# Kernel optimization log

Hardware: AMD Instinct MI355X
Metric: run time of the kernel (lower is better)

The kernel has to match this reference:

```python
import jax, jax.numpy as jnp
import numpy as np

N = 50000      # num nodes
E = 800000     # num edges (avg degree 16)
LAGS = 16      # in_channels of the cell input
FILT = 64      # hidden filters
K = 2          # diffusion steps
CIN = LAGS + FILT  # DConv input channels (cat of x and hidden)


def _dconv(X, row, col, norm_out, norm_in, W, b):
    """Diffusion conv, K=2. W: (2, K, Cin, Cout), b: (Cout,).
    Hop 0: identity for both directions. Hop 1: out-diffusion (D_O^-1 A) and
    in-diffusion (D_I^-1 A^T) via gather-scale-scatter."""
    H = X @ W[0, 0] + X @ W[1, 0]
    # out-direction: message along edge (row -> col), aggregated at col
    Tx_o = jax.ops.segment_sum(norm_out[:, None] * X[row], col, num_segments=N)
    # in-direction: reversed edges (col -> row), aggregated at row
    Tx_i = jax.ops.segment_sum(norm_in[:, None] * X[col], row, num_segments=N)
    H = H + Tx_o @ W[0, 1] + Tx_i @ W[1, 1]
    return H + b


def setup_inputs() -> dict:
    key = jax.random.key(0)
    ks = jax.random.split(key, 12)
    scale = 1.0 / np.sqrt(CIN)
    inp = {
        "x": jax.random.normal(ks[0], (N, LAGS), dtype=jnp.float32),
        "edge_index": jax.random.randint(ks[1], (2, E), 0, N, dtype=jnp.int64),
        "edge_weight": jax.random.uniform(ks[2], (E,), dtype=jnp.float32),
        "w_z": jax.random.uniform(ks[3], (2, K, CIN, FILT), jnp.float32, -scale, scale),
        "b_z": jnp.zeros((FILT,), jnp.float32),
        "w_r": jax.random.uniform(ks[4], (2, K, CIN, FILT), jnp.float32, -scale, scale),
        "b_r": jnp.zeros((FILT,), jnp.float32),
        "w_h": jax.random.uniform(ks[5], (2, K, CIN, FILT), jnp.float32, -scale, scale),
        "b_h": jnp.zeros((FILT,), jnp.float32),
        "lin_w": jax.random.uniform(ks[6], (FILT, 1), jnp.float32, -1.0 / np.sqrt(FILT), 1.0 / np.sqrt(FILT)),
        "lin_b": jnp.zeros((1,), jnp.float32),
    }
    return inp


def reference(x, edge_index, edge_weight, w_z, b_z, w_r, b_r, w_h, b_h, lin_w, lin_b):
    row, col = edge_index[0], edge_index[1]
    # weighted out/in degrees (original builds a dense adj just for these)
    deg_out = jax.ops.segment_sum(edge_weight, row, num_segments=N)
    deg_in = jax.ops.segment_sum(edge_weight, col, num_segments=N)
    deg_out = jnp.where(deg_out > 0, deg_out, 1.0)  # unused entries guarded
    deg_in = jnp.where(deg_in > 0, deg_in, 1.0)
    norm_out = (1.0 / deg_out)[row]
    norm_in = (1.0 / deg_in)[col]

    H0 = jnp.zeros((x.shape[0], FILT), dtype=x.dtype)  # hidden state init
    XH = jnp.concatenate([x, H0], axis=1)
    Z = jax.nn.sigmoid(_dconv(XH, row, col, norm_out, norm_in, w_z, b_z))
    R = jax.nn.sigmoid(_dconv(XH, row, col, norm_out, norm_in, w_r, b_r))
    XRH = jnp.concatenate([x, R * H0], axis=1)
    H_tilde = jnp.tanh(_dconv(XRH, row, col, norm_out, norm_in, w_h, b_h))
    H = Z * H0 + (1.0 - Z) * H_tilde
    h = jax.nn.relu(H)
    return h @ lin_w + lin_b  # [N, 1]
```

## Files before the change

kernel.cpp:

```cpp
#include <hip/hip_runtime.h>
#include <math.h>

#define N_NODES 50000
#define N_EDGES 800000
#define LAGS 16
#define FILT 64
#define W00_OFF 0
#define W01_OFF (80*64)
#define W10_OFF (2*80*64)
#define W11_OFF (3*80*64)

__device__ __forceinline__ void atomAddF(float* p, float v) {
    unsafeAtomicAdd(p, v);
}

__global__ __launch_bounds__(256) void deg_kernel(
    const int* __restrict__ row, const int* __restrict__ col,
    const float* __restrict__ ew,
    float* __restrict__ deg_out, float* __restrict__ deg_in)
{
    for (int e = blockIdx.x * 256 + threadIdx.x; e < N_EDGES;
         e += gridDim.x * 256) {
        float w = ew[e];
        atomAddF(&deg_out[row[e]], w);
        atomAddF(&deg_in[col[e]], w);
    }
}

__global__ __launch_bounds__(256) void scale_kernel(
    const float* __restrict__ x,
    const float* __restrict__ deg_out, const float* __restrict__ deg_in,
    float* __restrict__ Xs_o, float* __restrict__ Xs_i)
{
    for (int n = blockIdx.x * 256 + threadIdx.x; n < N_NODES;
         n += gridDim.x * 256) {
        float d_o = deg_out[n];
        float d_i = deg_in[n];
        float io = (d_o > 0.0f) ? (1.0f / d_o) : 1.0f;
        float ii = (d_i > 0.0f) ? (1.0f / d_i) : 1.0f;
        const float4* px = (const float4*)(x + (size_t)n * LAGS);
        float4* po = (float4*)(Xs_o + (size_t)n * LAGS);
        float4* pi = (float4*)(Xs_i + (size_t)n * LAGS);
#pragma unroll
        for (int q = 0; q < 4; ++q) {
            float4 v = px[q];
            po[q] = make_float4(io * v.x, io * v.y, io * v.z, io * v.w);
            pi[q] = make_float4(ii * v.x, ii * v.y, ii * v.z, ii * v.w);
        }
    }
}

__global__ __launch_bounds__(256) void scatter_kernel(
    const int* __restrict__ row, const int* __restrict__ col,
    const float* __restrict__ Xs_o, const float* __restrict__ Xs_i,
    float* __restrict__ Tx_o, float* __restrict__ Tx_i)
{
    const int total = N_EDGES * 16;
    for (int t = blockIdx.x * 256 + threadIdx.x; t < total;
         t += gridDim.x * 256) {
        int e  = t >> 4;
        int ch = t & 15;
        int r = row[e], c = col[e];
        float vo = Xs_o[(size_t)r * LAGS + ch];
        float vi = Xs_i[(size_t)c * LAGS + ch];
        atomAddF(&Tx_o[(size_t)c * LAGS + ch], vo);
        atomAddF(&Tx_i[(size_t)r * LAGS + ch], vi);
    }
}

__global__ __launch_bounds__(256) void node_kernel(
    const float* __restrict__ x,
    const float* __restrict__ Tx_o, const float* __restrict__ Tx_i,
    const float* __restrict__ w_z, const float* __restrict__ b_z,
    const float* __restrict__ w_h, const float* __restrict__ b_h,
    const float* __restrict__ lin_w, const float* __restrict__ lin_b,
    float* __restrict__ out)
{
    __shared__ float Wzc[FILT * 16], Wzo[FILT * 16], Wzi[FILT * 16];
    __shared__ float Whc[FILT * 16], Who[FILT * 16], Whi[FILT * 16];
    __shared__ float sbz[FILT], sbh[FILT], slw[FILT];

    const int tid = threadIdx.x;
    for (int i = tid; i < FILT * 16; i += 256) {
        int c = i >> 6, f = i & 63;
        int t = f * 16 + c;
        int g = c * 64 + f;
        Wzc[t] = w_z[W00_OFF + g] + w_z[W10_OFF + g];
        Wzo[t] = w_z[W01_OFF + g];
        Wzi[t] = w_z[W11_OFF + g];
        Whc[t] = w_h[W00_OFF + g] + w_h[W10_OFF + g];
        Who[t] = w_h[W01_OFF + g];
        Whi[t] = w_h[W11_OFF + g];
    }
    if (tid < FILT) {
        sbz[tid] = b_z[tid];
        sbh[tid] = b_h[tid];
        slw[tid] = lin_w[tid];
    }
    __syncthreads();

    int n = blockIdx.x * 256 + tid;
    if (n >= N_NODES) return;

    float v[48];
    {
        float4* vv = (float4*)v;
        const float4* px = (const float4*)(x    + (size_t)n * LAGS);
        const float4* po = (const float4*)(Tx_o + (size_t)n * LAGS);
        const float4* pi = (const float4*)(Tx_i + (size_t)n * LAGS);
#pragma unroll
        for (int q = 0; q < 4; ++q) {
            vv[q] = px[q]; vv[4 + q] = po[q]; vv[8 + q] = pi[q];
        }
    }

    float acc = 0.0f;
    for (int f = 0; f < FILT; ++f) {
        float az = sbz[f], ah = sbh[f];
        const float4* wzc = (const float4*)&Wzc[f * 16];
        const float4* wzo = (const float4*)&Wzo[f * 16];
        const float4* wzi = (const float4*)&Wzi[f * 16];
        const float4* whc = (const float4*)&Whc[f * 16];
        const float4* who = (const float4*)&Who[f * 16];
        const float4* whi = (const float4*)&Whi[f * 16];
#pragma unroll
        for (int q = 0; q < 4; ++q) {
            float4 a = wzc[q], b = wzo[q], cc = wzi[q];
            float4 d = whc[q], e = who[q], g = whi[q];
            const float* vx = &v[q * 4];
            const float* vo = &v[16 + q * 4];
            const float* vi = &v[32 + q * 4];
            az = fmaf(vx[0], a.x, az);  ah = fmaf(vx[0], d.x, ah);
            az = fmaf(vx[1], a.y, az);  ah = fmaf(vx[1], d.y, ah);
            az = fmaf(vx[2], a.z, az);  ah = fmaf(vx[2], d.z, ah);
            az = fmaf(vx[3], a.w, az);  ah = fmaf(vx[3], d.w, ah);
            az = fmaf(vo[0], b.x, az);  ah = fmaf(vo[0], e.x, ah);
            az = fmaf(vo[1], b.y, az);  ah = fmaf(vo[1], e.y, ah);
            az = fmaf(vo[2], b.z, az);  ah = fmaf(vo[2], e.z, ah);
            az = fmaf(vo[3], b.w, az);  ah = fmaf(vo[3], e.w, ah);
            az = fmaf(vi[0], cc.x, az); ah = fmaf(vi[0], g.x, ah);
            az = fmaf(vi[1], cc.y, az); ah = fmaf(vi[1], g.y, ah);
            az = fmaf(vi[2], cc.z, az); ah = fmaf(vi[2], g.z, ah);
            az = fmaf(vi[3], cc.w, az); ah = fmaf(vi[3], g.w, ah);
        }
        float z = 1.0f / (1.0f + __expf(-az));
        float th = 1.0f - 2.0f / (__expf(2.0f * ah) + 1.0f);
        acc = fmaf(fmaxf((1.0f - z) * th, 0.0f), slw[f], acc);
    }
    out[n] = acc + lin_b[0];
}

extern "C" void kernel_launch(void* const* d_in, const int* in_sizes, int n_in,
                              void* d_out, int out_size, void* d_ws, size_t ws_size,
                              hipStream_t stream)
{
    const float* x      = (const float*)d_in[0];
    const int*   eidx   = (const int*)d_in[1];
    const float* ew     = (const float*)d_in[2];
    const float* w_z    = (const float*)d_in[3];
    const float* b_z    = (const float*)d_in[4];
    const float* w_h    = (const float*)d_in[7];
    const float* b_h    = (const float*)d_in[8];
    const float* lin_w  = (const float*)d_in[9];
    const float* lin_b  = (const float*)d_in[10];
    float* out = (float*)d_out;

    const int* row = eidx;
    const int* col = eidx + N_EDGES;

    float* ws      = (float*)d_ws;
    float* deg_out = ws;
    float* deg_in  = ws + N_NODES;
    float* Tx_o    = ws + 2 * N_NODES;
    float* Tx_i    = ws + 2 * N_NODES + 16 * N_NODES;
    float* Xs_o    = ws + 2 * N_NODES + 32 * N_NODES;
    float* Xs_i    = ws + 2 * N_NODES + 48 * N_NODES;

    hipMemsetAsync(d_ws, 0, (size_t)(2 + 32) * N_NODES * sizeof(float), stream);

    int eb = 2048;
    deg_kernel<<<eb, 256, 0, stream>>>(row, col, ew, deg_out, deg_in);

    int nb = (N_NODES + 255) / 256;
    scale_kernel<<<nb, 256, 0, stream>>>(x, deg_out, deg_in, Xs_o, Xs_i);

    int sb = 2048;
    scatter_kernel<<<sb, 256, 0, stream>>>(row, col, Xs_o, Xs_i, Tx_o, Tx_i);

    node_kernel<<<nb, 256, 0, stream>>>(x, Tx_o, Tx_i, w_z, b_z, w_h, b_h,
                                        lin_w, lin_b, out);
}
```

Measured before the change: 287.4 us.

## Compute degrees with LDS-privatized partial histograms instead of global atomics

Replaces the global-atomic degree kernel with 128 blocks, each building a shared-memory histogram for one quarter of the node range over one edge slice and direction. The partial histograms are written out and summed per node inside the scale kernel. The workspace is reused, so the memset for the scatter accumulators now runs after the degree reduction. This removes contended global atomics on the degree arrays, but each block reads its whole edge slice and keeps only a quarter, so index reads are repeated and the grid of 128 blocks is small.

```diff
diff --git a/kernel.cpp b/kernel.cpp
--- a/kernel.cpp
+++ b/kernel.cpp
@@ -5,6 +5,8 @@
 #define N_EDGES 800000
 #define LAGS 16
 #define FILT 64
+#define QSIZE 12500
+#define NSLICE 16
 #define W00_OFF 0
 #define W01_OFF (80*64)
 #define W10_OFF (2*80*64)
@@ -14,39 +16,57 @@
     unsafeAtomicAdd(p, v);
 }
 
-__global__ __launch_bounds__(256) void deg_kernel(
+__global__ __launch_bounds__(256) void hist_kernel(
     const int* __restrict__ row, const int* __restrict__ col,
     const float* __restrict__ ew,
-    float* __restrict__ deg_out, float* __restrict__ deg_in)
-{
-    for (int e = blockIdx.x * 256 + threadIdx.x; e < N_EDGES;
-         e += gridDim.x * 256) {
+    float* __restrict__ part)
+{
+    __shared__ float hist[QSIZE];
+    const int b   = blockIdx.x;
+    const int dir = b >> 6;
+    const int q   = (b >> 4) & 3;
+    const int s   = b & 15;
+    const int* __restrict__ idx = dir ? col : row;
+
+    for (int i = threadIdx.x; i < QSIZE; i += 256) hist[i] = 0.0f;
+    __syncthreads();
+
+    const int ebase = s * (N_EDGES / NSLICE);
+    const int qbase = q * QSIZE;
+    for (int e = ebase + threadIdx.x; e < ebase + N_EDGES / NSLICE; e += 256) {
+        int n = idx[e];
         float w = ew[e];
-        atomAddF(&deg_out[row[e]], w);
-        atomAddF(&deg_in[col[e]], w);
-    }
-}
-
-__global__ __launch_bounds__(256) void scale_kernel(
-    const float* __restrict__ x,
-    const float* __restrict__ deg_out, const float* __restrict__ deg_in,
+        unsigned u = (unsigned)(n - qbase);
+        if (u < QSIZE) atomicAdd(&hist[u], w);
+    }
+    __syncthreads();
+
+    float* dst = part + (size_t)(dir * NSLICE + s) * N_NODES + qbase;
+    for (int i = threadIdx.x; i < QSIZE; i += 256) dst[i] = hist[i];
+}
+
+__global__ __launch_bounds__(256) void reduce_scale_kernel(
+    const float* __restrict__ part, const float* __restrict__ x,
     float* __restrict__ Xs_o, float* __restrict__ Xs_i)
 {
-    for (int n = blockIdx.x * 256 + threadIdx.x; n < N_NODES;
-         n += gridDim.x * 256) {
-        float d_o = deg_out[n];
-        float d_i = deg_in[n];
-        float io = (d_o > 0.0f) ? (1.0f / d_o) : 1.0f;
-        float ii = (d_i > 0.0f) ? (1.0f / d_i) : 1.0f;
-        const float4* px = (const float4*)(x + (size_t)n * LAGS);
-        float4* po = (float4*)(Xs_o + (size_t)n * LAGS);
-        float4* pi = (float4*)(Xs_i + (size_t)n * LAGS);
-#pragma unroll
-        for (int q = 0; q < 4; ++q) {
-            float4 v = px[q];
-            po[q] = make_float4(io * v.x, io * v.y, io * v.z, io * v.w);
-            pi[q] = make_float4(ii * v.x, ii * v.y, ii * v.z, ii * v.w);
-        }
+    int n = blockIdx.x * 256 + threadIdx.x;
+    if (n >= N_NODES) return;
+    float so = 0.0f, si = 0.0f;
+#pragma unroll
+    for (int s = 0; s < NSLICE; ++s) {
+        so += part[(size_t)s * N_NODES + n];
+        si += part[(size_t)(NSLICE + s) * N_NODES + n];
+    }
+    float io = (so > 0.0f) ? (1.0f / so) : 1.0f;
+    float ii = (si > 0.0f) ? (1.0f / si) : 1.0f;
+    const float4* px = (const float4*)(x + (size_t)n * LAGS);
+    float4* po = (float4*)(Xs_o + (size_t)n * LAGS);
+    float4* pi = (float4*)(Xs_i + (size_t)n * LAGS);
+#pragma unroll
+    for (int qq = 0; qq < 4; ++qq) {
+        float4 v = px[qq];
+        po[qq] = make_float4(io * v.x, io * v.y, io * v.z, io * v.w);
+        pi[qq] = make_float4(ii * v.x, ii * v.y, ii * v.z, ii * v.w);
     }
 }
 
@@ -168,24 +188,21 @@
     const int* row = eidx;
     const int* col = eidx + N_EDGES;
 
-    float* ws      = (float*)d_ws;
-    float* deg_out = ws;
-    float* deg_in  = ws + N_NODES;
-    float* Tx_o    = ws + 2 * N_NODES;
-    float* Tx_i    = ws + 2 * N_NODES + 16 * N_NODES;
-    float* Xs_o    = ws + 2 * N_NODES + 32 * N_NODES;
-    float* Xs_i    = ws + 2 * N_NODES + 48 * N_NODES;
-
-    hipMemsetAsync(d_ws, 0, (size_t)(2 + 32) * N_NODES * sizeof(float), stream);
-
-    int eb = 2048;
-    deg_kernel<<<eb, 256, 0, stream>>>(row, col, ew, deg_out, deg_in);
+    float* ws   = (float*)d_ws;
+    float* part = ws;
+    float* Tx_o = ws;
+    float* Tx_i = ws + 16 * N_NODES;
+    float* Xs_o = ws + 32 * N_NODES;
+    float* Xs_i = ws + 48 * N_NODES;
+
+    hist_kernel<<<128, 256, 0, stream>>>(row, col, ew, part);
 
     int nb = (N_NODES + 255) / 256;
-    scale_kernel<<<nb, 256, 0, stream>>>(x, deg_out, deg_in, Xs_o, Xs_i);
-
-    int sb = 2048;
-    scatter_kernel<<<sb, 256, 0, stream>>>(row, col, Xs_o, Xs_i, Tx_o, Tx_i);
+    reduce_scale_kernel<<<nb, 256, 0, stream>>>(part, x, Xs_o, Xs_i);
+
+    hipMemsetAsync(ws, 0, (size_t)32 * N_NODES * sizeof(float), stream);
+
+    scatter_kernel<<<2048, 256, 0, stream>>>(row, col, Xs_o, Xs_i, Tx_o, Tx_i);
 
     node_kernel<<<nb, 256, 0, stream>>>(x, Tx_o, Tx_i, w_z, b_z, w_h, b_h,
                                         lin_w, lin_b, out);
```

Result: slower. 307.4 us (+6.9%).

## Compute degrees with LDS-privatized histograms and fold Tx zeroing into scale

Applied to the files above, without the earlier changes.

Degree computation now uses LDS histograms: each block owns one direction, one node-range quarter and one edge slice. It accumulates weights into shared memory with LDS atomics, then flushes them to global with one atomic per bin. This is meant to cut global atomic traffic, but each edge index is now read by 8 different quarter blocks, so index reads rise eightfold. The Tx_o/Tx_i zeroing moves from the memset into the scale kernel, shrinking the memset to the degree arrays only.

```diff
diff --git a/kernel.cpp b/kernel.cpp
--- a/kernel.cpp
+++ b/kernel.cpp
@@ -5,6 +5,10 @@
 #define N_EDGES 800000
 #define LAGS 16
 #define FILT 64
+#define QSIZE 6250
+#define NQ 8
+#define NSLICE 32
+#define ESLICE (N_EDGES / NSLICE)
 #define W00_OFF 0
 #define W01_OFF (80*64)
 #define W10_OFF (2*80*64)
@@ -14,39 +18,62 @@
     unsafeAtomicAdd(p, v);
 }
 
-__global__ __launch_bounds__(256) void deg_kernel(
+__global__ __launch_bounds__(256) void hist_kernel(
     const int* __restrict__ row, const int* __restrict__ col,
     const float* __restrict__ ew,
     float* __restrict__ deg_out, float* __restrict__ deg_in)
 {
-    for (int e = blockIdx.x * 256 + threadIdx.x; e < N_EDGES;
-         e += gridDim.x * 256) {
+    __shared__ float hist[QSIZE];
+    const int b   = blockIdx.x;
+    const int dir = b >> 8;
+    const int q   = (b >> 5) & 7;
+    const int s   = b & 31;
+    const int* __restrict__ idx = dir ? col : row;
+
+    for (int i = threadIdx.x; i < QSIZE; i += 256) hist[i] = 0.0f;
+    __syncthreads();
+
+    const int ebase = s * ESLICE;
+    const int qbase = q * QSIZE;
+#pragma unroll 4
+    for (int e = ebase + threadIdx.x; e < ebase + ESLICE; e += 256) {
+        int n = idx[e];
         float w = ew[e];
-        atomAddF(&deg_out[row[e]], w);
-        atomAddF(&deg_in[col[e]], w);
-    }
+        unsigned u = (unsigned)(n - qbase);
+        if (u < QSIZE) atomAddF(&hist[u], w);
+    }
+    __syncthreads();
+
+    float* dst = (dir ? deg_in : deg_out) + qbase;
+    for (int i = threadIdx.x; i < QSIZE; i += 256)
+        atomAddF(&dst[i], hist[i]);
 }
 
 __global__ __launch_bounds__(256) void scale_kernel(
     const float* __restrict__ x,
     const float* __restrict__ deg_out, const float* __restrict__ deg_in,
-    float* __restrict__ Xs_o, float* __restrict__ Xs_i)
-{
-    for (int n = blockIdx.x * 256 + threadIdx.x; n < N_NODES;
-         n += gridDim.x * 256) {
-        float d_o = deg_out[n];
-        float d_i = deg_in[n];
-        float io = (d_o > 0.0f) ? (1.0f / d_o) : 1.0f;
-        float ii = (d_i > 0.0f) ? (1.0f / d_i) : 1.0f;
-        const float4* px = (const float4*)(x + (size_t)n * LAGS);
-        float4* po = (float4*)(Xs_o + (size_t)n * LAGS);
-        float4* pi = (float4*)(Xs_i + (size_t)n * LAGS);
+    float* __restrict__ Xs_o, float* __restrict__ Xs_i,
+    float* __restrict__ Tx_o, float* __restrict__ Tx_i)
+{
+    int n = blockIdx.x * 256 + threadIdx.x;
+    if (n >= N_NODES) return;
+    float d_o = deg_out[n];
+    float d_i = deg_in[n];
+    float io = (d_o > 0.0f) ? (1.0f / d_o) : 1.0f;
+    float ii = (d_i > 0.0f) ? (1.0f / d_i) : 1.0f;
+    const float4* px = (const float4*)(x + (size_t)n * LAGS);
+    float4* po = (float4*)(Xs_o + (size_t)n * LAGS);
+    float4* pi = (float4*)(Xs_i + (size_t)n * LAGS);
+    float4* zo = (float4*)(Tx_o + (size_t)n * LAGS);
+    float4* zi = (float4*)(Tx_i + (size_t)n * LAGS);
+    const float4 zero = make_float4(0.f, 0.f, 0.f, 0.f);
 #pragma unroll
-        for (int q = 0; q < 4; ++q) {
-            float4 v = px[q];
-            po[q] = make_float4(io * v.x, io * v.y, io * v.z, io * v.w);
-            pi[q] = make_float4(ii * v.x, ii * v.y, ii * v.z, ii * v.w);
-        }
+    for (int q = 0; q < 4; ++q) {
+        float4 v = px[q];
+        po[q] = make_float4(io * v.x, io * v.y, io * v.z, io * v.w);
+        pi[q] = make_float4(ii * v.x, ii * v.y, ii * v.z, ii * v.w);
+        zo[q] = zero;
+        zi[q] = zero;
     }
 }
 
@@ -176,16 +203,16 @@
     float* Xs_o    = ws + 2 * N_NODES + 32 * N_NODES;
     float* Xs_i    = ws + 2 * N_NODES + 48 * N_NODES;
 
-    hipMemsetAsync(d_ws, 0, (size_t)(2 + 32) * N_NODES * sizeof(float), stream);
-
-    int eb = 2048;
-    deg_kernel<<<eb, 256, 0, stream>>>(row, col, ew, deg_out, deg_in);
+    hipMemsetAsync(ws, 0, (size_t)2 * N_NODES * sizeof(float), stream);
+
+    hist_kernel<<<2 * NQ * NSLICE, 256, 0, stream>>>(row, col, ew,
+                                                     deg_out, deg_in);
 
     int nb = (N_NODES + 255) / 256;
-    scale_kernel<<<nb, 256, 0, stream>>>(x, deg_out, deg_in, Xs_o, Xs_i);
-
-    int sb = 2048;
-    scatter_kernel<<<sb, 256, 0, stream>>>(row, col, Xs_o, Xs_i, Tx_o, Tx_i);
+    scale_kernel<<<nb, 256, 0, stream>>>(x, deg_out, deg_in,
+                                         Xs_o, Xs_i, Tx_o, Tx_i);
+
+    scatter_kernel<<<2048, 256, 0, stream>>>(row, col, Xs_o, Xs_i, Tx_o, Tx_i);
 
     node_kernel<<<nb, 256, 0, stream>>>(x, Tx_o, Tx_i, w_z, b_z, w_h, b_h,
                                         lin_w, lin_b, out);
```

After: 264.6 us. 1.09x faster.

## Spread degree atomics across 8 slots and fold normalization into scatter

Applied to the files above, without the earlier changes.

Degree accumulation now writes into 8 per-node slots chosen by edge index, which spreads out atomic contention. A small kernel sums the slots and stores inverse degrees. The scale kernel and its pre-scaled feature copies are removed, so the scatter kernel reads raw x and multiplies by the inverse degree per edge. In exchange, the memset grows (8x degree buffers), each scatter thread does extra inverse-degree loads, and summation order changes slightly.

```diff
diff --git a/kernel.cpp b/kernel.cpp
--- a/kernel.cpp
+++ b/kernel.cpp
@@ -17,42 +17,32 @@
 __global__ __launch_bounds__(256) void deg_kernel(
     const int* __restrict__ row, const int* __restrict__ col,
     const float* __restrict__ ew,
-    float* __restrict__ deg_out, float* __restrict__ deg_in)
+    float* __restrict__ dw_out, float* __restrict__ dw_in)
 {
     for (int e = blockIdx.x * 256 + threadIdx.x; e < N_EDGES;
          e += gridDim.x * 256) {
         float w = ew[e];
-        atomAddF(&deg_out[row[e]], w);
-        atomAddF(&deg_in[col[e]], w);
+        int slot = e & 7;
+        atomAddF(&dw_out[(size_t)row[e] * 8 + slot], w);
+        atomAddF(&dw_in [(size_t)col[e] * 8 + slot], w);
     }
 }
 
-__global__ __launch_bounds__(256) void scale_kernel(
-    const float* __restrict__ x,
-    const float* __restrict__ deg_out, const float* __restrict__ deg_in,
-    float* __restrict__ Xs_o, float* __restrict__ Xs_i)
+__global__ __launch_bounds__(256) void inv_kernel(
+    const float* __restrict__ dw, float* __restrict__ inv)
 {
-    for (int n = blockIdx.x * 256 + threadIdx.x; n < N_NODES;
-         n += gridDim.x * 256) {
-        float d_o = deg_out[n];
-        float d_i = deg_in[n];
-        float io = (d_o > 0.0f) ? (1.0f / d_o) : 1.0f;
-        float ii = (d_i > 0.0f) ? (1.0f / d_i) : 1.0f;
-        const float4* px = (const float4*)(x + (size_t)n * LAGS);
-        float4* po = (float4*)(Xs_o + (size_t)n * LAGS);
-        float4* pi = (float4*)(Xs_i + (size_t)n * LAGS);
-#pragma unroll
-        for (int q = 0; q < 4; ++q) {
-            float4 v = px[q];
-            po[q] = make_float4(io * v.x, io * v.y, io * v.z, io * v.w);
-            pi[q] = make_float4(ii * v.x, ii * v.y, ii * v.z, ii * v.w);
-        }
-    }
+    int i = blockIdx.x * 256 + threadIdx.x;
+    if (i >= 2 * N_NODES) return;
+    const float4* p = (const float4*)(dw + (size_t)i * 8);
+    float4 a = p[0], b = p[1];
+    float d = ((a.x + a.y) + (a.z + a.w)) + ((b.x + b.y) + (b.z + b.w));
+    inv[i] = (d > 0.0f) ? (1.0f / d) : 1.0f;
 }
 
 __global__ __launch_bounds__(256) void scatter_kernel(
     const int* __restrict__ row, const int* __restrict__ col,
-    const float* __restrict__ Xs_o, const float* __restrict__ Xs_i,
+    const float* __restrict__ x,
+    const float* __restrict__ inv_out, const float* __restrict__ inv_in,
     float* __restrict__ Tx_o, float* __restrict__ Tx_i)
 {
     const int total = N_EDGES * 16;
@@ -61,10 +51,12 @@
         int e  = t >> 4;
         int ch = t & 15;
         int r = row[e], c = col[e];
-        float vo = Xs_o[(size_t)r * LAGS + ch];
-        float vi = Xs_i[(size_t)c * LAGS + ch];
-        atomAddF(&Tx_o[(size_t)c * LAGS + ch], vo);
-        atomAddF(&Tx_i[(size_t)r * LAGS + ch], vi);
+        float io = inv_out[r];
+        float ii = inv_in[c];
+        float xr = x[(size_t)r * LAGS + ch];
+        float xc = x[(size_t)c * LAGS + ch];
+        atomAddF(&Tx_o[(size_t)c * LAGS + ch], xr * io);
+        atomAddF(&Tx_i[(size_t)r * LAGS + ch], xc * ii);
     }
 }
 
@@ -168,25 +160,24 @@
     const int* row = eidx;
     const int* col = eidx + N_EDGES;
 
-    float* ws      = (float*)d_ws;
-    float* deg_out = ws;
-    float* deg_in  = ws + N_NODES;
-    float* Tx_o    = ws + 2 * N_NODES;
-    float* Tx_i    = ws + 2 * N_NODES + 16 * N_NODES;
-    float* Xs_o    = ws + 2 * N_NODES + 32 * N_NODES;
-    float* Xs_i    = ws + 2 * N_NODES + 48 * N_NODES;
+    float* ws     = (float*)d_ws;
+    float* dw_out = ws;
+    float* dw_in  = ws + 8 * N_NODES;
+    float* Tx_o   = ws + 16 * N_NODES;
+    float* Tx_i   = ws + 32 * N_NODES;
+    float* inv    = ws + 48 * N_NODES;
 
-    hipMemsetAsync(d_ws, 0, (size_t)(2 + 32) * N_NODES * sizeof(float), stream);
+    hipMemsetAsync(ws, 0, (size_t)48 * N_NODES * sizeof(float), stream);
 
-    int eb = 2048;
-    deg_kernel<<<eb, 256, 0, stream>>>(row, col, ew, deg_out, deg_in);
+    deg_kernel<<<2048, 256, 0, stream>>>(row, col, ew, dw_out, dw_in);
+
+    int ib = (2 * N_NODES + 255) / 256;
+    inv_kernel<<<ib, 256, 0, stream>>>(dw_out, inv);
+
+    scatter_kernel<<<2048, 256, 0, stream>>>(row, col, x,
+                                             inv, inv + N_NODES, Tx_o, Tx_i);
 
     int nb = (N_NODES + 255) / 256;
-    scale_kernel<<<nb, 256, 0, stream>>>(x, deg_out, deg_in, Xs_o, Xs_i);
-
-    int sb = 2048;
-    scatter_kernel<<<sb, 256, 0, stream>>>(row, col, Xs_o, Xs_i, Tx_o, Tx_i);
-
     node_kernel<<<nb, 256, 0, stream>>>(x, Tx_o, Tx_i, w_z, b_z, w_h, b_h,
                                         lin_w, lin_b, out);
 }
```

Result: no change. 282.8 us (-1.6%).
